# Optimization experiments

Measured on AMD Instinct MI355X. Metric: run time of the kernel, lower is better.

## Reference

```python
import jax, jax.numpy as jnp
import numpy as np

H = 1024      # hidden_size
V = 50257     # output_size (vocab)
L = 512       # max_length (encoder steps)


def setup_inputs() -> dict:
    key = jax.random.key(0)
    ks = jax.random.split(key, 12)
    s = 0.02
    return {
        "input": jax.random.randint(ks[0], (1,), 0, V),
        "h": jax.random.normal(ks[1], (1, 1, H), dtype=jnp.float32),
        "c": jax.random.normal(ks[2], (1, 1, H), dtype=jnp.float32),
        "encoder_outputs": jax.random.normal(ks[3], (L, H), dtype=jnp.float32),
        "emb_table": jax.random.normal(ks[4], (V, H), dtype=jnp.float32) * s,
        "W_attn": jax.random.normal(ks[5], (L, 2 * H), dtype=jnp.float32) * s,
        "b_attn": jnp.zeros((L,), jnp.float32),
        "W_comb": jax.random.normal(ks[6], (H, 2 * H), dtype=jnp.float32) * s,
        "b_comb": jnp.zeros((H,), jnp.float32),
        "W_ih": jax.random.normal(ks[7], (4 * H, H), dtype=jnp.float32) * s,
        "W_hh": jax.random.normal(ks[8], (4 * H, H), dtype=jnp.float32) * s,
        "b_ih": jnp.zeros((4 * H,), jnp.float32),
        "b_hh": jnp.zeros((4 * H,), jnp.float32),
        "W_out": jax.random.normal(ks[9], (V, H), dtype=jnp.float32) * s,
        "b_out": jnp.zeros((V,), jnp.float32),
    }


def reference(input, h, c, encoder_outputs, emb_table, W_attn, b_attn,
              W_comb, b_comb, W_ih, W_hh, b_ih, b_hh, W_out, b_out):
    # Single decode step, batch=1. Dropout is identity (eval mode).
    embedded = emb_table[input]            # [1, H]
    h0 = h[0]                              # [1, H]
    c0 = c[0]                              # [1, H]

    # attention over encoder outputs
    attn_logits = jnp.concatenate([embedded, h0], axis=1) @ W_attn.T + b_attn  # [1, L]
    attn_weights = jax.nn.softmax(attn_logits, axis=1)                          # [1, L]
    attn_applied = attn_weights @ encoder_outputs                               # [1, H]

    # combine + relu
    x = jnp.concatenate([embedded, attn_applied], axis=1) @ W_comb.T + b_comb   # [1, H]
    x = jax.nn.relu(x)

    # single-step LSTM cell (PyTorch gate order: i, f, g, o)
    gates = x @ W_ih.T + b_ih + h0 @ W_hh.T + b_hh                              # [1, 4H]
    i_g, f_g, g_g, o_g = jnp.split(gates, 4, axis=1)
    c1 = jax.nn.sigmoid(f_g) * c0 + jax.nn.sigmoid(i_g) * jnp.tanh(g_g)
    h1 = jax.nn.sigmoid(o_g) * jnp.tanh(c1)

    # output projection + log-softmax
    logp = jax.nn.log_softmax(h1 @ W_out.T + b_out, axis=1)                     # [1, V]
    return (logp, h1[None], c1[None], attn_weights)
```

## Files before the change

### kernel.cpp

```cpp
#include <hip/hip_runtime.h>
#include <math.h>

#define H 1024
#define V 50257
#define L 512
#define RBLK 64

__device__ __forceinline__ float wave_sum(float v) {
#pragma unroll
    for (int off = 32; off; off >>= 1) v += __shfl_xor(v, off, 64);
    return v;
}
__device__ __forceinline__ float wave_max(float v) {
#pragma unroll
    for (int off = 32; off; off >>= 1) v = fmaxf(v, __shfl_xor(v, off, 64));
    return v;
}
__device__ __forceinline__ float sigmoidf(float x) { return 1.f / (1.f + expf(-x)); }

__global__ void k_attn_logits(const int* __restrict__ inp, const float* __restrict__ h0,
                              const float* __restrict__ emb_table,
                              const float* __restrict__ W_attn, const float* __restrict__ b_attn,
                              float* __restrict__ logits) {
    int wave = (blockIdx.x * blockDim.x + threadIdx.x) >> 6;
    int lane = threadIdx.x & 63;
    if (wave >= L) return;
    const float* emb = emb_table + (size_t)inp[0] * H;
    const float* wrow = W_attn + (size_t)wave * (2 * H);
    float acc = 0.f;
#pragma unroll
    for (int it = 0; it < 8; ++it) {
        int k = it * 256 + lane * 4;
        float4 wv = *(const float4*)(wrow + k);
        const float* src = (k < H) ? (emb + k) : (h0 + (k - H));
        float4 xv = *(const float4*)src;
        acc += wv.x * xv.x + wv.y * xv.y + wv.z * xv.z + wv.w * xv.w;
    }
    acc = wave_sum(acc);
    if (lane == 0) logits[wave] = acc + b_attn[wave];
}

__global__ void k_softmax(const float* __restrict__ logits, float* __restrict__ attn_w,
                          float* __restrict__ ws_aa) {
    __shared__ float sh[8];
    __shared__ float bc;
    int t = threadIdx.x, lane = t & 63, wid = t >> 6;
    float v = logits[t];
    float m = wave_max(v);
    if (lane == 0) sh[wid] = m;
    __syncthreads();
    if (t == 0) { float mm = sh[0]; for (int i = 1; i < 8; ++i) mm = fmaxf(mm, sh[i]); bc = mm; }
    __syncthreads();
    m = bc;
    float e = expf(v - m);
    float s = wave_sum(e);
    __syncthreads();
    if (lane == 0) sh[wid] = s;
    __syncthreads();
    if (t == 0) { float ss = 0.f; for (int i = 0; i < 8; ++i) ss += sh[i]; bc = ss; }
    __syncthreads();
    attn_w[t] = e / bc;
    ws_aa[t] = 0.f;
    ws_aa[t + 512] = 0.f;
}

__global__ void k_attn_applied(const float* __restrict__ attn_w, const float* __restrict__ enc,
                               float* __restrict__ ws_aa) {
    int b = blockIdx.x, t = threadIdx.x;
    float4 acc = make_float4(0.f, 0.f, 0.f, 0.f);
#pragma unroll
    for (int r = 0; r < 8; ++r) {
        int l = b * 8 + r;
        float w = attn_w[l];
        float4 e = *(const float4*)(enc + (size_t)l * H + t * 4);
        acc.x += w * e.x; acc.y += w * e.y; acc.z += w * e.z; acc.w += w * e.w;
    }
    atomicAdd(&ws_aa[t * 4 + 0], acc.x);
    atomicAdd(&ws_aa[t * 4 + 1], acc.y);
    atomicAdd(&ws_aa[t * 4 + 2], acc.z);
    atomicAdd(&ws_aa[t * 4 + 3], acc.w);
}

__global__ void k_comb(const int* __restrict__ inp, const float* __restrict__ emb_table,
                       const float* __restrict__ ws_aa, const float* __restrict__ W_comb,
                       const float* __restrict__ b_comb, float* __restrict__ ws_x) {
    int wave = (blockIdx.x * blockDim.x + threadIdx.x) >> 6;
    int lane = threadIdx.x & 63;
    if (wave >= H) return;
    const float* emb = emb_table + (size_t)inp[0] * H;
    const float* wrow = W_comb + (size_t)wave * (2 * H);
    float acc = 0.f;
#pragma unroll
    for (int it = 0; it < 8; ++it) {
        int k = it * 256 + lane * 4;
        float4 wv = *(const float4*)(wrow + k);
        const float* src = (k < H) ? (emb + k) : (ws_aa + (k - H));
        float4 xv = *(const float4*)src;
        acc += wv.x * xv.x + wv.y * xv.y + wv.z * xv.z + wv.w * xv.w;
    }
    acc = wave_sum(acc);
    if (lane == 0) ws_x[wave] = fmaxf(acc + b_comb[wave], 0.f);
}

__global__ void k_gates_lstm(const float* __restrict__ ws_x, const float* __restrict__ h0,
                             const float* __restrict__ c0,
                             const float* __restrict__ W_ih, const float* __restrict__ W_hh,
                             const float* __restrict__ b_ih, const float* __restrict__ b_hh,
                             float* __restrict__ out_h1, float* __restrict__ out_c1) {
    __shared__ float g[4];
    int j = blockIdx.x;
    int wv = threadIdx.x >> 6;
    int lane = threadIdx.x & 63;
    int row = wv * H + j;
    const float* wi = W_ih + (size_t)row * H;
    const float* wh = W_hh + (size_t)row * H;
    float acc = 0.f;
#pragma unroll
    for (int it = 0; it < 4; ++it) {
        int k = it * 256 + lane * 4;
        float4 a = *(const float4*)(wi + k);
        float4 xv = *(const float4*)(ws_x + k);
        acc += a.x * xv.x + a.y * xv.y + a.z * xv.z + a.w * xv.w;
        float4 b = *(const float4*)(wh + k);
        float4 hv = *(const float4*)(h0 + k);
        acc += b.x * hv.x + b.y * hv.y + b.z * hv.z + b.w * hv.w;
    }
    acc = wave_sum(acc);
    if (lane == 0) g[wv] = acc + b_ih[row] + b_hh[row];
    __syncthreads();
    if (threadIdx.x == 0) {
        float ig = sigmoidf(g[0]);
        float fg = sigmoidf(g[1]);
        float gg = tanhf(g[2]);
        float og = sigmoidf(g[3]);
        float c1 = fg * c0[j] + ig * gg;
        out_c1[j] = c1;
        out_h1[j] = og * tanhf(c1);
    }
}

__global__ void k_out(const float* __restrict__ h1, const float* __restrict__ W_out,
                      const float* __restrict__ b_out, float* __restrict__ logp) {
    int wave = (blockIdx.x * blockDim.x + threadIdx.x) >> 6;
    int lane = threadIdx.x & 63;
    if (wave >= V) return;
    const float* wrow = W_out + (size_t)wave * H;
    float acc = 0.f;
#pragma unroll
    for (int it = 0; it < 4; ++it) {
        int k = it * 256 + lane * 4;
        float4 wv = *(const float4*)(wrow + k);
        float4 hv = *(const float4*)(h1 + k);
        acc += wv.x * hv.x + wv.y * hv.y + wv.z * hv.z + wv.w * hv.w;
    }
    acc = wave_sum(acc);
    if (lane == 0) logp[wave] = acc + b_out[wave];
}

__global__ void k_red(const float* __restrict__ logp, float* __restrict__ pair) {
    __shared__ float sh[4];
    int t = threadIdx.x, lane = t & 63, wid = t >> 6;
    float vals[4];
    int n = 0;
    float m = -1e30f;
    for (int v = blockIdx.x * 256 + t; v < V; v += RBLK * 256) {
        vals[n] = logp[v];
        m = fmaxf(m, vals[n]);
        ++n;
    }
    m = wave_max(m);
    if (lane == 0) sh[wid] = m;
    __syncthreads();
    float m4 = fmaxf(fmaxf(sh[0], sh[1]), fmaxf(sh[2], sh[3]));
    float s = 0.f;
    for (int i = 0; i < n; ++i) s += expf(vals[i] - m4);
    s = wave_sum(s);
    __syncthreads();
    if (lane == 0) sh[wid] = s;
    __syncthreads();
    if (t == 0) {
        pair[blockIdx.x * 2]     = m4;
        pair[blockIdx.x * 2 + 1] = sh[0] + sh[1] + sh[2] + sh[3];
    }
}

__global__ void k_sub(float* __restrict__ logp, const float* __restrict__ pair) {
    float mg = -1e30f;
#pragma unroll
    for (int i = 0; i < RBLK; ++i) mg = fmaxf(mg, pair[2 * i]);
    float sg = 0.f;
#pragma unroll
    for (int i = 0; i < RBLK; ++i) sg += pair[2 * i + 1] * expf(pair[2 * i] - mg);
    float lse = mg + logf(sg);
    int v = blockIdx.x * blockDim.x + threadIdx.x;
    if (v < V) logp[v] -= lse;
}

extern "C" void kernel_launch(void* const* d_in, const int* in_sizes, int n_in,
                              void* d_out, int out_size, void* d_ws, size_t ws_size,
                              hipStream_t stream) {
    const int*   inp     = (const int*)d_in[0];
    const float* h0      = (const float*)d_in[1];
    const float* c0      = (const float*)d_in[2];
    const float* enc     = (const float*)d_in[3];
    const float* emb     = (const float*)d_in[4];
    const float* W_attn  = (const float*)d_in[5];
    const float* b_attn  = (const float*)d_in[6];
    const float* W_comb  = (const float*)d_in[7];
    const float* b_comb  = (const float*)d_in[8];
    const float* W_ih    = (const float*)d_in[9];
    const float* W_hh    = (const float*)d_in[10];
    const float* b_ih    = (const float*)d_in[11];
    const float* b_hh    = (const float*)d_in[12];
    const float* W_out   = (const float*)d_in[13];
    const float* b_out   = (const float*)d_in[14];

    float* out      = (float*)d_out;
    float* out_logp = out;
    float* out_h1   = out + V;
    float* out_c1   = out + V + H;
    float* out_attn = out + V + 2 * H;

    float* ws        = (float*)d_ws;
    float* ws_logits = ws;
    float* ws_aa     = ws + 512;
    float* ws_x      = ws + 512 + 1024;
    float* ws_pair   = ws + 512 + 2048;

    k_attn_logits<<<128, 256, 0, stream>>>(inp, h0, emb, W_attn, b_attn, ws_logits);
    k_softmax<<<1, 512, 0, stream>>>(ws_logits, out_attn, ws_aa);
    k_attn_applied<<<64, 256, 0, stream>>>(out_attn, enc, ws_aa);
    k_comb<<<256, 256, 0, stream>>>(inp, emb, ws_aa, W_comb, b_comb, ws_x);
    k_gates_lstm<<<1024, 256, 0, stream>>>(ws_x, h0, c0, W_ih, W_hh, b_ih, b_hh, out_h1, out_c1);
    k_out<<<(V + 3) / 4, 256, 0, stream>>>(out_h1, W_out, b_out, out_logp);
    k_red<<<RBLK, 256, 0, stream>>>(out_logp, ws_pair);
    k_sub<<<(V + 255) / 256, 256, 0, stream>>>(out_logp, ws_pair);
}
```

Before: 433.7 us.

## Fuse attention, combine and LSTM stages into one persistent kernel with grid barriers

Replaces five separate front-end launches (attn logits, softmax, attn-applied, combine, LSTM gates) with a single 256-block kernel that uses atomic-counter grid barriers between phases. Softmax is recomputed redundantly per block so attention weights feed the weighted sum without a separate launch. The aim is to cut kernel launch and inter-kernel gaps on a latency-bound batch-1 step. It adds a memset launch and relies on all 256 blocks being co-resident for the spin barrier to avoid deadlock.

```diff
diff --git a/kernel.cpp b/kernel.cpp
--- a/kernel.cpp
+++ b/kernel.cpp
@@ -4,6 +4,7 @@
 #define H 1024
 #define V 50257
 #define L 512
+#define NB 256
 #define RBLK 64
 
 __device__ __forceinline__ float wave_sum(float v) {
@@ -18,124 +19,136 @@
 }
 __device__ __forceinline__ float sigmoidf(float x) { return 1.f / (1.f + expf(-x)); }
 
-__global__ void k_attn_logits(const int* __restrict__ inp, const float* __restrict__ h0,
-                              const float* __restrict__ emb_table,
-                              const float* __restrict__ W_attn, const float* __restrict__ b_attn,
-                              float* __restrict__ logits) {
-    int wave = (blockIdx.x * blockDim.x + threadIdx.x) >> 6;
-    int lane = threadIdx.x & 63;
-    if (wave >= L) return;
+__device__ __forceinline__ void gbar(int* cnt, int gen) {
+    __syncthreads();
+    if (threadIdx.x == 0) {
+        __threadfence();
+        atomicAdd(cnt, 1);
+        while (__hip_atomic_load(cnt, __ATOMIC_ACQUIRE, __HIP_MEMORY_SCOPE_AGENT) < gen * NB) {
+            __builtin_amdgcn_s_sleep(1);
+        }
+        __threadfence();
+    }
+    __syncthreads();
+}
+
+__global__ void __launch_bounds__(256) k_frontend(
+        const int* __restrict__ inp, const float* __restrict__ h0,
+        const float* __restrict__ c0, const float* __restrict__ emb_table,
+        const float* __restrict__ W_attn, const float* __restrict__ b_attn,
+        const float* __restrict__ enc,
+        const float* __restrict__ W_comb, const float* __restrict__ b_comb,
+        const float* __restrict__ W_ih, const float* __restrict__ W_hh,
+        const float* __restrict__ b_ih, const float* __restrict__ b_hh,
+        float* __restrict__ ws_logits, float* __restrict__ ws_aa,
+        float* __restrict__ ws_x, int* __restrict__ cnt,
+        float* __restrict__ out_attn, float* __restrict__ out_h1,
+        float* __restrict__ out_c1) {
+    const int t = threadIdx.x, lane = t & 63, wid = t >> 6;
+    const int gw = blockIdx.x * 4 + wid;
     const float* emb = emb_table + (size_t)inp[0] * H;
-    const float* wrow = W_attn + (size_t)wave * (2 * H);
-    float acc = 0.f;
-#pragma unroll
-    for (int it = 0; it < 8; ++it) {
-        int k = it * 256 + lane * 4;
-        float4 wv = *(const float4*)(wrow + k);
-        const float* src = (k < H) ? (emb + k) : (h0 + (k - H));
-        float4 xv = *(const float4*)src;
-        acc += wv.x * xv.x + wv.y * xv.y + wv.z * xv.z + wv.w * xv.w;
-    }
-    acc = wave_sum(acc);
-    if (lane == 0) logits[wave] = acc + b_attn[wave];
-}
-
-__global__ void k_softmax(const float* __restrict__ logits, float* __restrict__ attn_w,
-                          float* __restrict__ ws_aa) {
-    __shared__ float sh[8];
-    __shared__ float bc;
-    int t = threadIdx.x, lane = t & 63, wid = t >> 6;
-    float v = logits[t];
-    float m = wave_max(v);
-    if (lane == 0) sh[wid] = m;
-    __syncthreads();
-    if (t == 0) { float mm = sh[0]; for (int i = 1; i < 8; ++i) mm = fmaxf(mm, sh[i]); bc = mm; }
-    __syncthreads();
-    m = bc;
-    float e = expf(v - m);
-    float s = wave_sum(e);
-    __syncthreads();
-    if (lane == 0) sh[wid] = s;
-    __syncthreads();
-    if (t == 0) { float ss = 0.f; for (int i = 0; i < 8; ++i) ss += sh[i]; bc = ss; }
-    __syncthreads();
-    attn_w[t] = e / bc;
-    ws_aa[t] = 0.f;
-    ws_aa[t + 512] = 0.f;
-}
-
-__global__ void k_attn_applied(const float* __restrict__ attn_w, const float* __restrict__ enc,
-                               float* __restrict__ ws_aa) {
-    int b = blockIdx.x, t = threadIdx.x;
-    float4 acc = make_float4(0.f, 0.f, 0.f, 0.f);
-#pragma unroll
-    for (int r = 0; r < 8; ++r) {
-        int l = b * 8 + r;
-        float w = attn_w[l];
-        float4 e = *(const float4*)(enc + (size_t)l * H + t * 4);
-        acc.x += w * e.x; acc.y += w * e.y; acc.z += w * e.z; acc.w += w * e.w;
-    }
-    atomicAdd(&ws_aa[t * 4 + 0], acc.x);
-    atomicAdd(&ws_aa[t * 4 + 1], acc.y);
-    atomicAdd(&ws_aa[t * 4 + 2], acc.z);
-    atomicAdd(&ws_aa[t * 4 + 3], acc.w);
-}
-
-__global__ void k_comb(const int* __restrict__ inp, const float* __restrict__ emb_table,
-                       const float* __restrict__ ws_aa, const float* __restrict__ W_comb,
-                       const float* __restrict__ b_comb, float* __restrict__ ws_x) {
-    int wave = (blockIdx.x * blockDim.x + threadIdx.x) >> 6;
-    int lane = threadIdx.x & 63;
-    if (wave >= H) return;
-    const float* emb = emb_table + (size_t)inp[0] * H;
-    const float* wrow = W_comb + (size_t)wave * (2 * H);
-    float acc = 0.f;
-#pragma unroll
-    for (int it = 0; it < 8; ++it) {
-        int k = it * 256 + lane * 4;
-        float4 wv = *(const float4*)(wrow + k);
-        const float* src = (k < H) ? (emb + k) : (ws_aa + (k - H));
-        float4 xv = *(const float4*)src;
-        acc += wv.x * xv.x + wv.y * xv.y + wv.z * xv.z + wv.w * xv.w;
-    }
-    acc = wave_sum(acc);
-    if (lane == 0) ws_x[wave] = fmaxf(acc + b_comb[wave], 0.f);
-}
-
-__global__ void k_gates_lstm(const float* __restrict__ ws_x, const float* __restrict__ h0,
-                             const float* __restrict__ c0,
-                             const float* __restrict__ W_ih, const float* __restrict__ W_hh,
-                             const float* __restrict__ b_ih, const float* __restrict__ b_hh,
-                             float* __restrict__ out_h1, float* __restrict__ out_c1) {
-    __shared__ float g[4];
-    int j = blockIdx.x;
-    int wv = threadIdx.x >> 6;
-    int lane = threadIdx.x & 63;
-    int row = wv * H + j;
-    const float* wi = W_ih + (size_t)row * H;
-    const float* wh = W_hh + (size_t)row * H;
-    float acc = 0.f;
-#pragma unroll
-    for (int it = 0; it < 4; ++it) {
-        int k = it * 256 + lane * 4;
-        float4 a = *(const float4*)(wi + k);
-        float4 xv = *(const float4*)(ws_x + k);
-        acc += a.x * xv.x + a.y * xv.y + a.z * xv.z + a.w * xv.w;
-        float4 b = *(const float4*)(wh + k);
-        float4 hv = *(const float4*)(h0 + k);
-        acc += b.x * hv.x + b.y * hv.y + b.z * hv.z + b.w * hv.w;
-    }
-    acc = wave_sum(acc);
-    if (lane == 0) g[wv] = acc + b_ih[row] + b_hh[row];
-    __syncthreads();
-    if (threadIdx.x == 0) {
-        float ig = sigmoidf(g[0]);
-        float fg = sigmoidf(g[1]);
-        float gg = tanhf(g[2]);
-        float og = sigmoidf(g[3]);
-        float c1 = fg * c0[j] + ig * gg;
-        out_c1[j] = c1;
-        out_h1[j] = og * tanhf(c1);
+    __shared__ float sh[4];
+    __shared__ float g4[4][4];
+
+    if (gw < L) {
+        const float* wrow = W_attn + (size_t)gw * (2 * H);
+        float acc = 0.f;
+#pragma unroll
+        for (int it = 0; it < 8; ++it) {
+            int k = it * 256 + lane * 4;
+            float4 wv = *(const float4*)(wrow + k);
+            const float* src = (k < H) ? (emb + k) : (h0 + (k - H));
+            float4 xv = *(const float4*)src;
+            acc += wv.x * xv.x + wv.y * xv.y + wv.z * xv.z + wv.w * xv.w;
+        }
+        acc = wave_sum(acc);
+        if (lane == 0) ws_logits[gw] = acc + b_attn[gw];
+    } else if (gw < L + 16) {
+        ws_aa[(gw - L) * 64 + lane] = 0.f;
+    }
+    gbar(cnt, 1);
+
+    if (blockIdx.x <= 64) {
+        float v0 = ws_logits[t], v1 = ws_logits[t + 256];
+        float m = wave_max(fmaxf(v0, v1));
+        if (lane == 0) sh[wid] = m;
+        __syncthreads();
+        m = fmaxf(fmaxf(sh[0], sh[1]), fmaxf(sh[2], sh[3]));
+        float e0 = expf(v0 - m), e1 = expf(v1 - m);
+        float s = wave_sum(e0 + e1);
+        __syncthreads();
+        if (lane == 0) sh[wid] = s;
+        __syncthreads();
+        s = sh[0] + sh[1] + sh[2] + sh[3];
+        if (blockIdx.x == 64) {
+            out_attn[t] = e0 / s;
+            out_attn[t + 256] = e1 / s;
+        } else {
+            int b = blockIdx.x;
+            float4 acc = make_float4(0.f, 0.f, 0.f, 0.f);
+#pragma unroll
+            for (int r = 0; r < 8; ++r) {
+                int l = b * 8 + r;
+                float w = expf(ws_logits[l] - m) / s;
+                float4 e = *(const float4*)(enc + (size_t)l * H + t * 4);
+                acc.x += w * e.x; acc.y += w * e.y; acc.z += w * e.z; acc.w += w * e.w;
+            }
+            atomicAdd(&ws_aa[t * 4 + 0], acc.x);
+            atomicAdd(&ws_aa[t * 4 + 1], acc.y);
+            atomicAdd(&ws_aa[t * 4 + 2], acc.z);
+            atomicAdd(&ws_aa[t * 4 + 3], acc.w);
+        }
+    }
+    gbar(cnt, 2);
+
+    {
+        const float* wrow = W_comb + (size_t)gw * (2 * H);
+        float acc = 0.f;
+#pragma unroll
+        for (int it = 0; it < 8; ++it) {
+            int k = it * 256 + lane * 4;
+            float4 wv = *(const float4*)(wrow + k);
+            const float* src = (k < H) ? (emb + k) : (ws_aa + (k - H));
+            float4 xv = *(const float4*)src;
+            acc += wv.x * xv.x + wv.y * xv.y + wv.z * xv.z + wv.w * xv.w;
+        }
+        acc = wave_sum(acc);
+        if (lane == 0) ws_x[gw] = fmaxf(acc + b_comb[gw], 0.f);
+    }
+    gbar(cnt, 3);
+
+    {
+        int jbase = blockIdx.x * 4;
+#pragma unroll
+        for (int i = 0; i < 4; ++i) {
+            int row = wid * H + jbase + i;
+            const float* wi = W_ih + (size_t)row * H;
+            const float* wh = W_hh + (size_t)row * H;
+            float acc = 0.f;
+#pragma unroll
+            for (int it = 0; it < 4; ++it) {
+                int k = it * 256 + lane * 4;
+                float4 a = *(const float4*)(wi + k);
+                float4 xv = *(const float4*)(ws_x + k);
+                acc += a.x * xv.x + a.y * xv.y + a.z * xv.z + a.w * xv.w;
+                float4 bb = *(const float4*)(wh + k);
+                float4 hv = *(const float4*)(h0 + k);
+                acc += bb.x * hv.x + bb.y * hv.y + bb.z * hv.z + bb.w * hv.w;
+            }
+            acc = wave_sum(acc);
+            if (lane == 0) g4[wid][i] = acc + b_ih[row] + b_hh[row];
+        }
+        __syncthreads();
+        if (t < 4) {
+            int j = jbase + t;
+            float ig = sigmoidf(g4[0][t]);
+            float fg = sigmoidf(g4[1][t]);
+            float gg = tanhf(g4[2][t]);
+            float og = sigmoidf(g4[3][t]);
+            float c1 = fg * c0[j] + ig * gg;
+            out_c1[j] = c1;
+            out_h1[j] = og * tanhf(c1);
+        }
     }
 }
 
@@ -222,16 +235,17 @@
     float* out_attn = out + V + 2 * H;
 
     float* ws        = (float*)d_ws;
-    float* ws_logits = ws;
-    float* ws_aa     = ws + 512;
-    float* ws_x      = ws + 512 + 1024;
-    float* ws_pair   = ws + 512 + 2048;
-
-    k_attn_logits<<<128, 256, 0, stream>>>(inp, h0, emb, W_attn, b_attn, ws_logits);
-    k_softmax<<<1, 512, 0, stream>>>(ws_logits, out_attn, ws_aa);
-    k_attn_applied<<<64, 256, 0, stream>>>(out_attn, enc, ws_aa);
-    k_comb<<<256, 256, 0, stream>>>(inp, emb, ws_aa, W_comb, b_comb, ws_x);
-    k_gates_lstm<<<1024, 256, 0, stream>>>(ws_x, h0, c0, W_ih, W_hh, b_ih, b_hh, out_h1, out_c1);
+    int*   ws_cnt    = (int*)d_ws;
+    float* ws_logits = ws + 64;
+    float* ws_aa     = ws + 64 + 512;
+    float* ws_x      = ws + 64 + 512 + 1024;
+    float* ws_pair   = ws + 64 + 512 + 2048;
+
+    hipMemsetAsync(d_ws, 0, 256, stream);
+    k_frontend<<<NB, 256, 0, stream>>>(inp, h0, c0, emb, W_attn, b_attn, enc,
+                                       W_comb, b_comb, W_ih, W_hh, b_ih, b_hh,
+                                       ws_logits, ws_aa, ws_x, ws_cnt,
+                                       out_attn, out_h1, out_c1);
     k_out<<<(V + 3) / 4, 256, 0, stream>>>(out_h1, W_out, b_out, out_logp);
     k_red<<<RBLK, 256, 0, stream>>>(out_logp, ws_pair);
     k_sub<<<(V + 255) / 256, 256, 0, stream>>>(out_logp, ws_pair);
```

New measurement: 482.3 us. 1.11x slower.
